# Performance work log

Measured on AMD Instinct MI355X. Metric: run time of the kernel, lower is better.

## Reference

```python
import jax, jax.numpy as jnp
import numpy as np

B, N, DIM, H, DH = 4, 16384, 256, 8, 32
INNER = H * DH
SCALE = DH ** -0.5


def setup_inputs() -> dict:
    key = jax.random.key(0)
    ks = jax.random.split(key, 15)
    g = lambda k, shape, s=0.02: jax.random.normal(k, shape, dtype=jnp.float32) * s
    return {
        "states": jax.random.normal(ks[0], (B, N, DIM), dtype=jnp.float32),
        "agent_qs": jax.random.normal(ks[1], (B, N, DIM), dtype=jnp.float32),
        "obs": jax.random.normal(ks[2], (B, N, DIM), dtype=jnp.float32),
        "Wq": g(ks[3], (DIM, INNER)), "bq": g(ks[4], (INNER,)),
        "Wk": g(ks[5], (DIM, INNER)), "bk": g(ks[6], (INNER,)),
        "Wv": g(ks[7], (DIM, INNER)), "bv": g(ks[8], (INNER,)),
        "wq_attn": g(ks[9], (DH,), 0.1),
        "wk_attn": g(ks[10], (DH,), 0.1),
        "Wr": g(ks[11], (DH, DH)), "br": g(ks[12], (DH,)),
        "Wout": g(ks[13], (INNER, DIM)), "bout": g(ks[14], (DIM,)),
    }


def _heads(t):
    # [b, n, h*d] -> [b, h, n, d]
    b, n, _ = t.shape
    return t.reshape(b, n, H, DH).transpose(0, 2, 1, 3)


def reference(states, agent_qs, obs, Wq, bq, Wk, bk, Wv, bv,
              wq_attn, wk_attn, Wr, br, Wout, bout):
    q = _heads(jnp.abs(states @ Wq + bq))   # b h n d
    k = _heads(agent_qs @ Wk + bk)          # b h n d
    v = _heads(obs @ Wv + bv)               # b h n d

    # additive attention pooling for global query
    q_attn = jax.nn.softmax(jnp.einsum('bhnd,d->bhn', q, wq_attn) * SCALE, axis=-1)
    global_q = jnp.einsum('bhn,bhnd->bhd', q_attn, q)  # b h d

    # gate keys with global query, pool against ORIGINAL k (k_aggr)
    k_gated = k * global_q[:, :, None, :]
    k_attn = jax.nn.softmax(jnp.einsum('bhnd,d->bhn', k_gated, wk_attn) * SCALE, axis=-1)
    global_k = jnp.einsum('bhn,bhnd->bhd', k_attn, k)  # b h d

    u = v * global_k[:, :, None, :]
    r = u @ Wr + br + q                      # b h n d
    r = r.transpose(0, 2, 1, 3).reshape(r.shape[0], r.shape[2], INNER)  # b n (h d)
    return r @ Wout + bout
```

## Files before the change

kernel.cpp:

```cpp
#include <hip/hip_runtime.h>
#include <hip/hip_bf16.h>

#define B_   4
#define N_   16384
#define T_   65536
static constexpr float SCALE_F = 0.17677669529663687f;

typedef __attribute__((ext_vector_type(8))) short bf16x8;
typedef __attribute__((ext_vector_type(4))) float f32x4;

#define BAR() __builtin_amdgcn_s_barrier()
#define WAIT(vm) asm volatile("s_waitcnt vmcnt(" #vm ") lgkmcnt(0)" ::: "memory")

static __device__ __forceinline__ unsigned pk2bf(float lo, float hi) {
    __hip_bfloat162 t = __float22bfloat162_rn(make_float2(lo, hi));
    union { __hip_bfloat162 h; unsigned u; } c; c.h = t; return c.u;
}
static __device__ __forceinline__ unsigned short f2bf(float f) {
    unsigned u = __float_as_uint(f);
    u += 0x7fffu + ((u >> 16) & 1u);
    return (unsigned short)(u >> 16);
}
static __device__ __forceinline__ void gl_lds16(const void* g, void* l) {
    __builtin_amdgcn_global_load_lds(
        (const __attribute__((address_space(1))) unsigned int*)g,
        (__attribute__((address_space(3))) unsigned int*)l, 16, 0, 0);
}

__global__ __launch_bounds__(256) void prep_all(
    const float* __restrict__ Wq, const float* __restrict__ Wk,
    const float* __restrict__ Wv, unsigned short* __restrict__ Wt,
    const float* __restrict__ Wr, const float* __restrict__ br,
    const float* __restrict__ Wout, const float* __restrict__ bout,
    float* __restrict__ S1t, float* __restrict__ cvec)
{
    const int blk = blockIdx.x;
    if (blk < 3) {
        const float* W = (blk == 0) ? Wq : (blk == 1) ? Wk : Wv;
        unsigned short* dst = Wt + (size_t)blk * 65536 + (size_t)threadIdx.x * 256;
        #pragma unroll 4
        for (int kb = 0; kb < 32; ++kb) {
            float v[8];
            #pragma unroll
            for (int e = 0; e < 8; ++e) v[e] = W[(kb*8 + e)*256 + threadIdx.x];
            uint4 w;
            w.x = pk2bf(v[0], v[1]); w.y = pk2bf(v[2], v[3]);
            w.z = pk2bf(v[4], v[5]); w.w = pk2bf(v[6], v[7]);
            *reinterpret_cast<uint4*>(dst + kb*8) = w;
        }
        return;
    }
    const int i = blk - 3, j = threadIdx.x;
    if (i < 256) {
        const int h = i >> 5, dd = i & 31;
        float s = 0.f;
        #pragma unroll 8
        for (int dp = 0; dp < 32; ++dp)
            s = fmaf(Wr[dd*32 + dp], Wout[(h*32 + dp)*256 + j], s);
        S1t[(size_t)j*256 + i] = s;
    } else {
        float cj = bout[j];
        for (int r = 0; r < 256; ++r) cj = fmaf(br[r & 31], Wout[r*256 + j], cj);
        cvec[j] = cj;
    }
}

__global__ __launch_bounds__(256) void proj_mfma(
    const float* __restrict__ states, const float* __restrict__ agent_qs,
    const float* __restrict__ obs, const unsigned short* __restrict__ Wt,
    const float* __restrict__ bq, const float* __restrict__ bk,
    const float* __restrict__ bv,
    unsigned short* __restrict__ q_bf, unsigned short* __restrict__ k_bf,
    unsigned short* __restrict__ v_bf)
{
    __shared__ __align__(16) float As[3][64*32];

    const int tid = threadIdx.x;
    const int z  = blockIdx.y;
    const int t0 = blockIdx.x * 64;

    const float* X = (z == 0) ? states : (z == 1) ? agent_qs : obs;
    const unsigned short* Bt = Wt + (size_t)z * 65536;
    const float* bias = (z == 0) ? bq : (z == 1) ? bk : bv;
    unsigned short* Y = (z == 0) ? q_bf : (z == 1) ? k_bf : v_bf;
    const bool doabs = (z == 0);

    const int wid = tid >> 6, lane = tid & 63;
    const int l15 = lane & 15, g = lane >> 4;
    const int wc = wid;

    int ntrue[4];
    #pragma unroll
    for (int ni = 0; ni < 4; ++ni) {
        int np = ni*16 + l15;
        int c = (np & 32) | ((np & 12) << 1) | ((np & 16) >> 2) | (np & 3);
        ntrue[ni] = wc*64 + c;
    }

    const int srow_lane = lane >> 3;
    const int schunk = (lane & 7) ^ (lane >> 3);
    auto stageA = [&](int buf, int step) {
        const int k0 = step * 32;
        #pragma unroll
        for (int i = 0; i < 2; ++i) {
            int r = (wid*2 + i)*8 + srow_lane;
            gl_lds16(X + (size_t)(t0 + r)*256 + k0 + schunk*4,
                     &As[buf][(wid*2 + i)*256]);
        }
    };
    auto loadB = [&](bf16x8* breg, int step) {
        const int k0 = step * 32;
        #pragma unroll
        for (int ni = 0; ni < 4; ++ni)
            breg[ni] = *reinterpret_cast<const bf16x8*>(
                Bt + (size_t)ntrue[ni]*256 + k0 + g*8);
    };
    auto dsreadA = [&](int buf, f32x4* lo, f32x4* hi) {
        #pragma unroll
        for (int mi = 0; mi < 4; ++mi) {
            int m = mi*16 + l15;
            int x = m & 7;
            lo[mi] = *reinterpret_cast<const f32x4*>(&As[buf][m*32 + ((2*g)  ^x)*4]);
            hi[mi] = *reinterpret_cast<const f32x4*>(&As[buf][m*32 + ((2*g+1)^x)*4]);
        }
    };

    f32x4 acc[4][4];
    #pragma unroll
    for (int mi = 0; mi < 4; ++mi)
        #pragma unroll
        for (int ni = 0; ni < 4; ++ni) acc[mi][ni] = (f32x4){0.f,0.f,0.f,0.f};

    auto mfma_step = [&](const bf16x8* bb, const f32x4* lo, const f32x4* hi) {
        bf16x8 a[4];
        #pragma unroll
        for (int mi = 0; mi < 4; ++mi) {
            union { unsigned u[4]; bf16x8 v; } cc;
            cc.u[0] = pk2bf(lo[mi][0], lo[mi][1]);
            cc.u[1] = pk2bf(lo[mi][2], lo[mi][3]);
            cc.u[2] = pk2bf(hi[mi][0], hi[mi][1]);
            cc.u[3] = pk2bf(hi[mi][2], hi[mi][3]);
            a[mi] = cc.v;
        }
        #pragma unroll
        for (int mi = 0; mi < 4; ++mi)
            #pragma unroll
            for (int ni = 0; ni < 4; ++ni)
                acc[mi][ni] = __builtin_amdgcn_mfma_f32_16x16x32_bf16(
                    bb[ni], a[mi], acc[mi][ni], 0, 0, 0);
    };

    bf16x8 bcur[4], bn[4];
    loadB(bcur, 0);
    stageA(0, 0);
    stageA(1, 1);
    WAIT(0); BAR();

    int br_ = 0, bw_ = 2;
    for (int s = 0; s < 6; ++s) {
        loadB(bn, s + 1);
        f32x4 lo[4], hi[4];
        dsreadA(br_, lo, hi);
        stageA(bw_, s + 2);
        mfma_step(bcur, lo, hi);
        WAIT(6); BAR();
        #pragma unroll
        for (int ni = 0; ni < 4; ++ni) bcur[ni] = bn[ni];
        br_ = (br_ == 2) ? 0 : br_ + 1;
        bw_ = (bw_ == 2) ? 0 : bw_ + 1;
    }
    {
        loadB(bn, 7);
        f32x4 lo[4], hi[4];
        dsreadA(br_, lo, hi);
        mfma_step(bcur, lo, hi);
        WAIT(4); BAR();
        #pragma unroll
        for (int ni = 0; ni < 4; ++ni) bcur[ni] = bn[ni];
        br_ = (br_ == 2) ? 0 : br_ + 1;
    }
    {
        f32x4 lo[4], hi[4];
        dsreadA(br_, lo, hi);
        mfma_step(bcur, lo, hi);
    }

    #pragma unroll
    for (int s = 0; s < 2; ++s) {
        int colb = wc*64 + s*32 + g*8;
        float4 b0 = *reinterpret_cast<const float4*>(bias + colb);
        float4 b1 = *reinterpret_cast<const float4*>(bias + colb + 4);
        #pragma unroll
        for (int mi = 0; mi < 4; ++mi) {
            int m = t0 + mi*16 + l15;
            float y0 = acc[mi][2*s  ][0] + b0.x;
            float y1 = acc[mi][2*s  ][1] + b0.y;
            float y2 = acc[mi][2*s  ][2] + b0.z;
            float y3 = acc[mi][2*s  ][3] + b0.w;
            float y4 = acc[mi][2*s+1][0] + b1.x;
            float y5 = acc[mi][2*s+1][1] + b1.y;
            float y6 = acc[mi][2*s+1][2] + b1.z;
            float y7 = acc[mi][2*s+1][3] + b1.w;
            if (doabs) {
                y0 = fabsf(y0); y1 = fabsf(y1); y2 = fabsf(y2); y3 = fabsf(y3);
                y4 = fabsf(y4); y5 = fabsf(y5); y6 = fabsf(y6); y7 = fabsf(y7);
            }
            uint4 pk;
            pk.x = pk2bf(y0, y1); pk.y = pk2bf(y2, y3);
            pk.z = pk2bf(y4, y5); pk.w = pk2bf(y6, y7);
            *reinterpret_cast<uint4*>(Y + (size_t)m*256 + colb) = pk;
        }
    }
}

__global__ __launch_bounds__(512) void pool_partial(
    const unsigned short* __restrict__ data,
    const float* __restrict__ wqa, const float* __restrict__ wka,
    const float* __restrict__ part_in, float* __restrict__ part_out, int mode)
{
    const int bh = blockIdx.x, ch = blockIdx.y;
    const int b = bh >> 3, h = bh & 7;
    const int tid = threadIdx.x;

    __shared__ float coef[32];
    __shared__ float s_red[8];
    __shared__ float a_red[8][32];

    if (tid < 32) {
        float cc;
        if (mode == 0) cc = wqa[tid];
        else {
            float num = 0.f, den = 0.f;
            #pragma unroll
            for (int c = 0; c < 8; ++c) {
                num += part_in[(size_t)(bh*8 + c)*40 + tid];
                den += part_in[(size_t)(bh*8 + c)*40 + 32];
            }
            cc = (num / den) * wka[tid];
        }
        coef[tid] = cc * SCALE_F;
    }
    __syncthreads();
    float cf[32];
    #pragma unroll
    for (int d = 0; d < 32; ++d) cf[d] = coef[d];

    float s = 0.f;
    float acc[32];
    #pragma unroll
    for (int d = 0; d < 32; ++d) acc[d] = 0.f;

    const unsigned short* base = data + (size_t)b * N_ * 256 + h * 32;
    for (int n = ch*2048 + tid; n < (ch + 1)*2048; n += 512) {
        const uint4* p = reinterpret_cast<const uint4*>(base + (size_t)n * 256);
        float qv[32];
        #pragma unroll
        for (int gg = 0; gg < 4; ++gg) {
            uint4 r = p[gg];
            unsigned w0 = r.x, w1 = r.y, w2 = r.z, w3 = r.w;
            qv[gg*8+0] = __uint_as_float(w0 << 16);
            qv[gg*8+1] = __uint_as_float(w0 & 0xffff0000u);
            qv[gg*8+2] = __uint_as_float(w1 << 16);
            qv[gg*8+3] = __uint_as_float(w1 & 0xffff0000u);
            qv[gg*8+4] = __uint_as_float(w2 << 16);
            qv[gg*8+5] = __uint_as_float(w2 & 0xffff0000u);
            qv[gg*8+6] = __uint_as_float(w3 << 16);
            qv[gg*8+7] = __uint_as_float(w3 & 0xffff0000u);
        }
        float l = 0.f;
        #pragma unroll
        for (int d = 0; d < 32; ++d) l = fmaf(qv[d], cf[d], l);
        float e = expf(l);
        s += e;
        #pragma unroll
        for (int d = 0; d < 32; ++d) acc[d] = fmaf(e, qv[d], acc[d]);
    }

    #pragma unroll
    for (int off = 1; off < 64; off <<= 1) {
        s += __shfl_xor(s, off);
        #pragma unroll
        for (int d = 0; d < 32; ++d) acc[d] += __shfl_xor(acc[d], off);
    }
    const int wave = tid >> 6, lane = tid & 63;
    if (lane == 0) {
        s_red[wave] = s;
        #pragma unroll
        for (int d = 0; d < 32; ++d) a_red[wave][d] = acc[d];
    }
    __syncthreads();
    if (tid < 32) {
        float num = 0.f, den = 0.f;
        #pragma unroll
        for (int w2 = 0; w2 < 8; ++w2) { num += a_red[w2][tid]; den += s_red[w2]; }
        part_out[(size_t)(bh*8 + ch)*40 + tid] = num;
        if (tid == 0) part_out[(size_t)(bh*8 + ch)*40 + 32] = den;
    }
}

__global__ __launch_bounds__(256) void build_wcat_t(
    const float* __restrict__ part_k, const float* __restrict__ S1t,
    const float* __restrict__ Wout, unsigned short* __restrict__ Wcat_t)
{
    const int b = blockIdx.x, n = blockIdx.y, k = threadIdx.x;
    const int h = k >> 5, d = k & 31;
    float num = 0.f, den = 0.f;
    #pragma unroll
    for (int c = 0; c < 8; ++c) {
        num += part_k[(size_t)((b*8 + h)*8 + c)*40 + d];
        den += part_k[(size_t)((b*8 + h)*8 + c)*40 + 32];
    }
    const float gkv = num / den;
    unsigned short* dst = Wcat_t + (size_t)(b*256 + n) * 512;
    dst[k]       = f2bf(gkv * S1t[(size_t)n*256 + k]);
    dst[k + 256] = f2bf(Wout[(size_t)k*256 + n]);
}

__global__ __launch_bounds__(256) void out_mfma(
    const unsigned short* __restrict__ v_bf, const unsigned short* __restrict__ q_bf,
    const unsigned short* __restrict__ Wcat_t, const float* __restrict__ cvec,
    float* __restrict__ out)
{
    __shared__ __align__(16) unsigned short As[3][64*32];

    const int tid = threadIdx.x;
    const int t0 = blockIdx.x * 64;
    const int b  = t0 >> 14;
    const unsigned short* Wb = Wcat_t + (size_t)b * 256 * 512;

    const int wid = tid >> 6, lane = tid & 63;
    const int l15 = lane & 15, g = lane >> 4, wc = wid;

    const int sr = wid*16 + (lane >> 2);
    const int stc = (lane & 3) ^ (sr & 3) ^ ((sr >> 2) & 3);
    auto stageA = [&](int buf, int step) {
        const int k0 = step * 32;
        const unsigned short* src = (k0 < 256) ? v_bf : q_bf;
        int ks = k0 & 255;
        gl_lds16(src + (size_t)(t0 + sr)*256 + ks + stc*8, &As[buf][wid*512]);
    };
    auto loadB = [&](bf16x8* breg, int step) {
        const int k0 = step * 32;
        #pragma unroll
        for (int ni = 0; ni < 4; ++ni) {
            int nt = wc*64 + ni*16 + l15;
            breg[ni] = *reinterpret_cast<const bf16x8*>(
                Wb + (size_t)nt*512 + k0 + g*8);
        }
    };

    f32x4 acc[4][4];
    #pragma unroll
    for (int mi = 0; mi < 4; ++mi)
        #pragma unroll
        for (int ni = 0; ni < 4; ++ni) acc[mi][ni] = (f32x4){0.f,0.f,0.f,0.f};

    auto step_body = [&](int buf, const bf16x8* bb) {
        bf16x8 a[4];
        #pragma unroll
        for (int mi = 0; mi < 4; ++mi) {
            int m = mi*16 + l15;
            int cc = g ^ (m & 3) ^ ((m >> 2) & 3);
            a[mi] = *reinterpret_cast<const bf16x8*>(&As[buf][m*32 + cc*8]);
        }
        #pragma unroll
        for (int mi = 0; mi < 4; ++mi)
            #pragma unroll
            for (int ni = 0; ni < 4; ++ni)
                acc[mi][ni] = __builtin_amdgcn_mfma_f32_16x16x32_bf16(
                    bb[ni], a[mi], acc[mi][ni], 0, 0, 0);
    };

    bf16x8 bcur[4], bn[4];
    loadB(bcur, 0);
    stageA(0, 0);
    stageA(1, 1);
    WAIT(0); BAR();

    int br_ = 0, bw_ = 2;
    for (int s = 0; s < 14; ++s) {
        loadB(bn, s + 1);
        stageA(bw_, s + 2);
        step_body(br_, bcur);
        WAIT(5); BAR();
        #pragma unroll
        for (int ni = 0; ni < 4; ++ni) bcur[ni] = bn[ni];
        br_ = (br_ == 2) ? 0 : br_ + 1;
        bw_ = (bw_ == 2) ? 0 : bw_ + 1;
    }
    {
        loadB(bn, 15);
        step_body(br_, bcur);
        WAIT(4); BAR();
        #pragma unroll
        for (int ni = 0; ni < 4; ++ni) bcur[ni] = bn[ni];
        br_ = (br_ == 2) ? 0 : br_ + 1;
    }
    step_body(br_, bcur);

    #pragma unroll
    for (int ni = 0; ni < 4; ++ni) {
        int colb = wc*64 + ni*16 + g*4;
        float4 cv = *reinterpret_cast<const float4*>(cvec + colb);
        #pragma unroll
        for (int mi = 0; mi < 4; ++mi) {
            int m = t0 + mi*16 + l15;
            float4 o;
            o.x = acc[mi][ni][0] + cv.x;
            o.y = acc[mi][ni][1] + cv.y;
            o.z = acc[mi][ni][2] + cv.z;
            o.w = acc[mi][ni][3] + cv.w;
            *reinterpret_cast<float4*>(out + (size_t)m*256 + colb) = o;
        }
    }
}

extern "C" void kernel_launch(void* const* d_in, const int* in_sizes, int n_in,
                              void* d_out, int out_size, void* d_ws, size_t ws_size,
                              hipStream_t stream)
{
    const float* states   = (const float*)d_in[0];
    const float* agent_qs = (const float*)d_in[1];
    const float* obs      = (const float*)d_in[2];
    const float* Wq   = (const float*)d_in[3];
    const float* bq   = (const float*)d_in[4];
    const float* Wk   = (const float*)d_in[5];
    const float* bk   = (const float*)d_in[6];
    const float* Wv   = (const float*)d_in[7];
    const float* bv   = (const float*)d_in[8];
    const float* wq_attn = (const float*)d_in[9];
    const float* wk_attn = (const float*)d_in[10];
    const float* Wr   = (const float*)d_in[11];
    const float* br   = (const float*)d_in[12];
    const float* Wout = (const float*)d_in[13];
    const float* bout = (const float*)d_in[14];
    float* out = (float*)d_out;

    char* w = (char*)d_ws;
    unsigned short* q_bf = (unsigned short*)w; w += (size_t)T_ * 256 * 2;
    unsigned short* k_bf = (unsigned short*)w; w += (size_t)T_ * 256 * 2;
    unsigned short* v_bf = (unsigned short*)w; w += (size_t)T_ * 256 * 2;
    unsigned short* Wt_bf   = (unsigned short*)w; w += (size_t)3 * 65536 * 2;
    unsigned short* Wcat_t  = (unsigned short*)w; w += (size_t)4 * 256 * 512 * 2;
    float* part_q = (float*)w; w += (size_t)256 * 40 * sizeof(float);
    float* part_k = (float*)w; w += (size_t)256 * 40 * sizeof(float);
    float* S1t  = (float*)w; w += (size_t)256 * 256 * sizeof(float);
    float* cvec = (float*)w; w += 256 * sizeof(float);

    prep_all<<<dim3(260), 256, 0, stream>>>(Wq, Wk, Wv, Wt_bf,
                                            Wr, br, Wout, bout, S1t, cvec);
    proj_mfma<<<dim3(1024, 3), 256, 0, stream>>>(
        states, agent_qs, obs, Wt_bf, bq, bk, bv, q_bf, k_bf, v_bf);
    pool_partial<<<dim3(32, 8), 512, 0, stream>>>(q_bf, wq_attn, wk_attn,
                                                  part_q, part_q, 0);
    pool_partial<<<dim3(32, 8), 512, 0, stream>>>(k_bf, wq_attn, wk_attn,
                                                  part_q, part_k, 1);
    build_wcat_t<<<dim3(4, 256), 256, 0, stream>>>(part_k, S1t, Wout, Wcat_t);
    out_mfma<<<dim3(1024), 256, 0, stream>>>(v_bf, q_bf, Wcat_t, cvec, out);
}
```

Baseline: 206.1 us.

## Replace LDS-staged pipelines with direct global loads in projection and output GEMMs

```diff
diff --git a/kernel.cpp b/kernel.cpp
--- a/kernel.cpp
+++ b/kernel.cpp
@@ -9,9 +9,6 @@
 typedef __attribute__((ext_vector_type(8))) short bf16x8;
 typedef __attribute__((ext_vector_type(4))) float f32x4;
 
-#define BAR() __builtin_amdgcn_s_barrier()
-#define WAIT(vm) asm volatile("s_waitcnt vmcnt(" #vm ") lgkmcnt(0)" ::: "memory")
-
 static __device__ __forceinline__ unsigned pk2bf(float lo, float hi) {
     __hip_bfloat162 t = __float22bfloat162_rn(make_float2(lo, hi));
     union { __hip_bfloat162 h; unsigned u; } c; c.h = t; return c.u;
@@ -20,11 +17,6 @@
     unsigned u = __float_as_uint(f);
     u += 0x7fffu + ((u >> 16) & 1u);
     return (unsigned short)(u >> 16);
-}
-static __device__ __forceinline__ void gl_lds16(const void* g, void* l) {
-    __builtin_amdgcn_global_load_lds(
-        (const __attribute__((address_space(1))) unsigned int*)g,
-        (__attribute__((address_space(3))) unsigned int*)l, 16, 0, 0);
 }
 
 __global__ __launch_bounds__(256) void prep_all(
@@ -73,8 +65,6 @@
     unsigned short* __restrict__ q_bf, unsigned short* __restrict__ k_bf,
     unsigned short* __restrict__ v_bf)
 {
-    __shared__ __align__(16) float As[3][64*32];
-
     const int tid = threadIdx.x;
     const int z  = blockIdx.y;
     const int t0 = blockIdx.x * 64;
@@ -89,57 +79,39 @@
     const int l15 = lane & 15, g = lane >> 4;
     const int wc = wid;
 
-    int ntrue[4];
+    const float* abase[4];
+    const unsigned short* bbase[4];
+    #pragma unroll
+    for (int mi = 0; mi < 4; ++mi)
+        abase[mi] = X + (size_t)(t0 + mi*16 + l15) * 256 + g*8;
     #pragma unroll
     for (int ni = 0; ni < 4; ++ni) {
         int np = ni*16 + l15;
         int c = (np & 32) | ((np & 12) << 1) | ((np & 16) >> 2) | (np & 3);
-        ntrue[ni] = wc*64 + c;
-    }
-
-    const int srow_lane = lane >> 3;
-    const int schunk = (lane & 7) ^ (lane >> 3);
-    auto stageA = [&](int buf, int step) {
-        const int k0 = step * 32;
-        #pragma unroll
-        for (int i = 0; i < 2; ++i) {
-            int r = (wid*2 + i)*8 + srow_lane;
-            gl_lds16(X + (size_t)(t0 + r)*256 + k0 + schunk*4,
-                     &As[buf][(wid*2 + i)*256]);
-        }
-    };
-    auto loadB = [&](bf16x8* breg, int step) {
-        const int k0 = step * 32;
+        bbase[ni] = Bt + (size_t)(wc*64 + c) * 256 + g*8;
+    }
+
+    f32x4 acc[4][4];
+    #pragma unroll
+    for (int mi = 0; mi < 4; ++mi)
+        #pragma unroll
+        for (int ni = 0; ni < 4; ++ni) acc[mi][ni] = (f32x4){0.f,0.f,0.f,0.f};
+
+    #pragma unroll
+    for (int kk = 0; kk < 8; ++kk) {
+        bf16x8 bb[4], a[4];
         #pragma unroll
         for (int ni = 0; ni < 4; ++ni)
-            breg[ni] = *reinterpret_cast<const bf16x8*>(
-                Bt + (size_t)ntrue[ni]*256 + k0 + g*8);
-    };
-    auto dsreadA = [&](int buf, f32x4* lo, f32x4* hi) {
+            bb[ni] = *reinterpret_cast<const bf16x8*>(bbase[ni] + kk*32);
         #pragma unroll
         for (int mi = 0; mi < 4; ++mi) {
-            int m = mi*16 + l15;
-            int x = m & 7;
-            lo[mi] = *reinterpret_cast<const f32x4*>(&As[buf][m*32 + ((2*g)  ^x)*4]);
-            hi[mi] = *reinterpret_cast<const f32x4*>(&As[buf][m*32 + ((2*g+1)^x)*4]);
-        }
-    };
-
-    f32x4 acc[4][4];
-    #pragma unroll
-    for (int mi = 0; mi < 4; ++mi)
-        #pragma unroll
-        for (int ni = 0; ni < 4; ++ni) acc[mi][ni] = (f32x4){0.f,0.f,0.f,0.f};
-
-    auto mfma_step = [&](const bf16x8* bb, const f32x4* lo, const f32x4* hi) {
-        bf16x8 a[4];
-        #pragma unroll
-        for (int mi = 0; mi < 4; ++mi) {
+            f32x4 lo = *reinterpret_cast<const f32x4*>(abase[mi] + kk*32);
+            f32x4 hi = *reinterpret_cast<const f32x4*>(abase[mi] + kk*32 + 4);
             union { unsigned u[4]; bf16x8 v; } cc;
-            cc.u[0] = pk2bf(lo[mi][0], lo[mi][1]);
-            cc.u[1] = pk2bf(lo[mi][2], lo[mi][3]);
-            cc.u[2] = pk2bf(hi[mi][0], hi[mi][1]);
-            cc.u[3] = pk2bf(hi[mi][2], hi[mi][3]);
+            cc.u[0] = pk2bf(lo[0], lo[1]);
+            cc.u[1] = pk2bf(lo[2], lo[3]);
+            cc.u[2] = pk2bf(hi[0], hi[1]);
+            cc.u[3] = pk2bf(hi[2], hi[3]);
             a[mi] = cc.v;
         }
         #pragma unroll
@@ -148,41 +120,6 @@
             for (int ni = 0; ni < 4; ++ni)
                 acc[mi][ni] = __builtin_amdgcn_mfma_f32_16x16x32_bf16(
                     bb[ni], a[mi], acc[mi][ni], 0, 0, 0);
-    };
-
-    bf16x8 bcur[4], bn[4];
-    loadB(bcur, 0);
-    stageA(0, 0);
-    stageA(1, 1);
-    WAIT(0); BAR();
-
-    int br_ = 0, bw_ = 2;
-    for (int s = 0; s < 6; ++s) {
-        loadB(bn, s + 1);
-        f32x4 lo[4], hi[4];
-        dsreadA(br_, lo, hi);
-        stageA(bw_, s + 2);
-        mfma_step(bcur, lo, hi);
-        WAIT(6); BAR();
-        #pragma unroll
-        for (int ni = 0; ni < 4; ++ni) bcur[ni] = bn[ni];
-        br_ = (br_ == 2) ? 0 : br_ + 1;
-        bw_ = (bw_ == 2) ? 0 : bw_ + 1;
-    }
-    {
-        loadB(bn, 7);
-        f32x4 lo[4], hi[4];
-        dsreadA(br_, lo, hi);
-        mfma_step(bcur, lo, hi);
-        WAIT(4); BAR();
-        #pragma unroll
-        for (int ni = 0; ni < 4; ++ni) bcur[ni] = bn[ni];
-        br_ = (br_ == 2) ? 0 : br_ + 1;
-    }
-    {
-        f32x4 lo[4], hi[4];
-        dsreadA(br_, lo, hi);
-        mfma_step(bcur, lo, hi);
     }
 
     #pragma unroll
@@ -321,8 +258,6 @@
     const unsigned short* __restrict__ Wcat_t, const float* __restrict__ cvec,
     float* __restrict__ out)
 {
-    __shared__ __align__(16) unsigned short As[3][64*32];
-
     const int tid = threadIdx.x;
     const int t0 = blockIdx.x * 64;
     const int b  = t0 >> 14;
@@ -331,23 +266,18 @@
     const int wid = tid >> 6, lane = tid & 63;
     const int l15 = lane & 15, g = lane >> 4, wc = wid;
 
-    const int sr = wid*16 + (lane >> 2);
-    const int stc = (lane & 3) ^ (sr & 3) ^ ((sr >> 2) & 3);
-    auto stageA = [&](int buf, int step) {
-        const int k0 = step * 32;
-        const unsigned short* src = (k0 < 256) ? v_bf : q_bf;
-        int ks = k0 & 255;
-        gl_lds16(src + (size_t)(t0 + sr)*256 + ks + stc*8, &As[buf][wid*512]);
-    };
-    auto loadB = [&](bf16x8* breg, int step) {
-        const int k0 = step * 32;
-        #pragma unroll
-        for (int ni = 0; ni < 4; ++ni) {
-            int nt = wc*64 + ni*16 + l15;
-            breg[ni] = *reinterpret_cast<const bf16x8*>(
-                Wb + (size_t)nt*512 + k0 + g*8);
-        }
-    };
+    const unsigned short* av[4];
+    const unsigned short* aq[4];
+    const unsigned short* bbase[4];
+    #pragma unroll
+    for (int mi = 0; mi < 4; ++mi) {
+        size_t row = (size_t)(t0 + mi*16 + l15) * 256 + g*8;
+        av[mi] = v_bf + row;
+        aq[mi] = q_bf + row;
+    }
+    #pragma unroll
+    for (int ni = 0; ni < 4; ++ni)
+        bbase[ni] = Wb + (size_t)(wc*64 + ni*16 + l15) * 512 + g*8;
 
     f32x4 acc[4][4];
     #pragma unroll
@@ -355,48 +285,38 @@
         #pragma unroll
         for (int ni = 0; ni < 4; ++ni) acc[mi][ni] = (f32x4){0.f,0.f,0.f,0.f};
 
-    auto step_body = [&](int buf, const bf16x8* bb) {
-        bf16x8 a[4];
-        #pragma unroll
-        for (int mi = 0; mi < 4; ++mi) {
-            int m = mi*16 + l15;
-            int cc = g ^ (m & 3) ^ ((m >> 2) & 3);
-            a[mi] = *reinterpret_cast<const bf16x8*>(&As[buf][m*32 + cc*8]);
-        }
+    #pragma unroll
+    for (int kk = 0; kk < 8; ++kk) {
+        bf16x8 a[4], bb[4];
+        #pragma unroll
+        for (int ni = 0; ni < 4; ++ni)
+            bb[ni] = *reinterpret_cast<const bf16x8*>(bbase[ni] + kk*32);
+        #pragma unroll
+        for (int mi = 0; mi < 4; ++mi)
+            a[mi] = *reinterpret_cast<const bf16x8*>(av[mi] + kk*32);
         #pragma unroll
         for (int mi = 0; mi < 4; ++mi)
             #pragma unroll
             for (int ni = 0; ni < 4; ++ni)
                 acc[mi][ni] = __builtin_amdgcn_mfma_f32_16x16x32_bf16(
                     bb[ni], a[mi], acc[mi][ni], 0, 0, 0);
-    };
-
-    bf16x8 bcur[4], bn[4];
-    loadB(bcur, 0);
-    stageA(0, 0);
-    stageA(1, 1);
-    WAIT(0); BAR();
-
-    int br_ = 0, bw_ = 2;
-    for (int s = 0; s < 14; ++s) {
-        loadB(bn, s + 1);
-        stageA(bw_, s + 2);
-        step_body(br_, bcur);
-        WAIT(5); BAR();
-        #pragma unroll
-        for (int ni = 0; ni < 4; ++ni) bcur[ni] = bn[ni];
-        br_ = (br_ == 2) ? 0 : br_ + 1;
-        bw_ = (bw_ == 2) ? 0 : bw_ + 1;
-    }
-    {
-        loadB(bn, 15);
-        step_body(br_, bcur);
-        WAIT(4); BAR();
-        #pragma unroll
-        for (int ni = 0; ni < 4; ++ni) bcur[ni] = bn[ni];
-        br_ = (br_ == 2) ? 0 : br_ + 1;
-    }
-    step_body(br_, bcur);
+    }
+    #pragma unroll
+    for (int kk = 8; kk < 16; ++kk) {
+        bf16x8 a[4], bb[4];
+        #pragma unroll
+        for (int ni = 0; ni < 4; ++ni)
+            bb[ni] = *reinterpret_cast<const bf16x8*>(bbase[ni] + kk*32);
+        #pragma unroll
+        for (int mi = 0; mi < 4; ++mi)
+            a[mi] = *reinterpret_cast<const bf16x8*>(aq[mi] + (kk-8)*32);
+        #pragma unroll
+        for (int mi = 0; mi < 4; ++mi)
+            #pragma unroll
+            for (int ni = 0; ni < 4; ++ni)
+                acc[mi][ni] = __builtin_amdgcn_mfma_f32_16x16x32_bf16(
+                    bb[ni], a[mi], acc[mi][ni], 0, 0, 0);
+    }
 
     #pragma unroll
     for (int ni = 0; ni < 4; ++ni) {
```

Result: slower. 290.2 us (+40.8%).
